# Optimization experiments

Hardware: AMD Instinct MI355X
Metric: run time of the kernel (lower is better)

Reference implementation:

```python
import jax, jax.numpy as jnp
import numpy as np

N_NODES, FEAT_DIM, EMBED_DIM, BATCH, N_NEIGH = 200000, 128, 64, 8192, 64


def setup_inputs() -> dict:
    key = jax.random.key(0)
    k0, k1, k2, k3, k4, k5 = jax.random.split(key, 6)
    return {
        "features_table": jax.random.normal(k0, (N_NODES, FEAT_DIM), jnp.float32),
        # xavier-uniform-like scale for [2*feat_dim, embed_dim]
        "weight": jax.random.normal(k1, (2 * FEAT_DIM, EMBED_DIM), jnp.float32)
        * (1.0 / np.sqrt(2 * FEAT_DIM)),
        "nodes": jax.random.randint(k2, (BATCH,), 0, N_NODES),
        "batch_scores": jax.random.normal(k3, (BATCH, 2), jnp.float32),
        "neigh_scores": jax.random.normal(k4, (BATCH, N_NEIGH, 2), jnp.float32),
        "neighs_ids": jax.random.randint(k5, (BATCH, N_NEIGH), 0, N_NODES),
        "num_sample": 16,
    }


def reference(features_table, weight, nodes, batch_scores, neigh_scores, neighs_ids, num_sample):
    # |center_score - neigh_score| per candidate neighbor  -> [B, K]
    score_diff = jnp.abs(batch_scores[:, :1] - neigh_scores[:, :, 0])
    # keep num_sample neighbors with SMALLEST score diff (top_k on negated diffs)
    neg_top, sel_idx = jax.lax.top_k(-score_diff, num_sample)  # [B, k]
    samp_scores = -neg_top  # selected (ascending-ish) score diffs, as in choose_step_test
    sel_ids = jnp.take_along_axis(neighs_ids, sel_idx, axis=1)  # [B, k]
    # masked-mean aggregation == mean of the k selected neighbor features
    neigh_feats = features_table[sel_ids]            # [B, k, F]
    agg_feats = neigh_feats.mean(axis=1)             # [B, F]
    self_feats = features_table[nodes]               # [B, F]
    cat_feats = jnp.concatenate([self_feats, agg_feats], axis=1)  # [B, 2F]
    to_feats = jax.nn.relu(cat_feats @ weight)       # [B, E]
    return to_feats, samp_scores
```

## Files before the change

### kernel.cpp

```cpp
#include <hip/hip_runtime.h>

#define BATCH   8192
#define NNEIGH  64
#define FEAT    128
#define EMBED   64
#define ROWS    8
#define CATP    260
#define EPAD    68
#define KCH     8

__global__ __launch_bounds__(256, 4) void intra_agg_kernel(
    const float* __restrict__ feat,
    const float* __restrict__ W,
    const int*   __restrict__ nodes,
    const float* __restrict__ bscore,
    const float* __restrict__ nscore,
    const int*   __restrict__ nids,
    const int*   __restrict__ ns_ptr,
    float*       __restrict__ out)
{
    const int b0   = blockIdx.x * ROWS;
    const int tid  = threadIdx.x;
    const int lane = tid & 63;
    const int wave = tid >> 6;
    const int ns   = *ns_ptr;

    __shared__ float s_cat[ROWS * CATP];
    __shared__ float s_part[KCH][ROWS][EPAD];

    const int r0   = wave * 2;
    const int half = lane >> 5;
    const int c    = lane & 31;

    const int    selfnode = nodes[b0 + r0 + half];
    const float4 self4    = *(const float4*)&feat[(size_t)selfnode * FEAT + c * 4];

    float d[2];
    int   idx[2];
    #pragma unroll
    for (int i = 0; i < 2; ++i) {
        const int row = b0 + r0 + i;
        const float  ctr = bscore[row * 2];
        const float2 sc  = *(const float2*)&nscore[(size_t)(row * NNEIGH + lane) * 2];
        d[i]   = fabsf(ctr - sc.x);
        idx[i] = lane;
    }
    #pragma unroll
    for (int k = 2; k <= 64; k <<= 1) {
        #pragma unroll
        for (int j = k >> 1; j > 0; j >>= 1) {
            #pragma unroll
            for (int i = 0; i < 2; ++i) {
                const float od = __shfl_xor(d[i], j);
                const int   oi = __shfl_xor(idx[i], j);
                const bool up    = ((lane & k) == 0);
                const bool lower = ((lane & j) == 0);
                const bool oless = (od < d[i]) || (od == d[i] && oi < idx[i]);
                if ((lower == up) ? oless : !oless) { d[i] = od; idx[i] = oi; }
            }
        }
    }
    int gid[2] = {0, 0};
    #pragma unroll
    for (int i = 0; i < 2; ++i) {
        const int row = b0 + r0 + i;
        if (lane < ns) {
            out[(size_t)BATCH * EMBED + (size_t)row * ns + lane] = d[i];
            gid[i] = nids[row * NNEIGH + idx[i]];
        }
    }

    float4 a = make_float4(0.f, 0.f, 0.f, 0.f);
    if (ns == 16) {
        #pragma unroll
        for (int j = 0; j < 16; ++j) {
            const int id0 = __shfl(gid[0], j);
            const int id1 = __shfl(gid[1], j);
            const int id  = half ? id1 : id0;
            const float4 v = *(const float4*)&feat[(size_t)id * FEAT + c * 4];
            a.x += v.x; a.y += v.y; a.z += v.z; a.w += v.w;
        }
    } else {
        for (int j = 0; j < ns; ++j) {
            const int id0 = __shfl(gid[0], j);
            const int id1 = __shfl(gid[1], j);
            const int id  = half ? id1 : id0;
            const float4 v = *(const float4*)&feat[(size_t)id * FEAT + c * 4];
            a.x += v.x; a.y += v.y; a.z += v.z; a.w += v.w;
        }
    }
    const float inv_ns = 1.0f / (float)ns;
    a.x *= inv_ns; a.y *= inv_ns; a.z *= inv_ns; a.w *= inv_ns;

    {
        const int r = r0 + half;
        *(float4*)&s_cat[r * CATP + c * 4]        = self4;
        *(float4*)&s_cat[r * CATP + FEAT + c * 4] = a;
    }
    __syncthreads();

    {
        const int q  = tid & 15;
        const int rq = (tid >> 4) & 1;
        const int ks = tid >> 5;
        const int k0 = ks * 32;

        float4 acc[4];
        #pragma unroll
        for (int r = 0; r < 4; ++r) acc[r] = make_float4(0.f, 0.f, 0.f, 0.f);

        #pragma unroll
        for (int kk = 0; kk < 32; kk += 4) {
            const int k = k0 + kk;
            float4 cv[4];
            #pragma unroll
            for (int r = 0; r < 4; ++r)
                cv[r] = *(const float4*)&s_cat[(rq * 4 + r) * CATP + k];
            #pragma unroll
            for (int t = 0; t < 4; ++t) {
                const float4 w4 = *(const float4*)&W[(size_t)(k + t) * EMBED + q * 4];
                #pragma unroll
                for (int r = 0; r < 4; ++r) {
                    const float cf = (t == 0) ? cv[r].x : (t == 1) ? cv[r].y
                                   : (t == 2) ? cv[r].z : cv[r].w;
                    acc[r].x += cf * w4.x; acc[r].y += cf * w4.y;
                    acc[r].z += cf * w4.z; acc[r].w += cf * w4.w;
                }
            }
        }
        #pragma unroll
        for (int r = 0; r < 4; ++r)
            *(float4*)&s_part[ks][rq * 4 + r][q * 4] = acc[r];
    }
    __syncthreads();

    if (tid < ROWS * 16) {
        const int r2 = tid >> 4;
        const int q  = tid & 15;
        float4 o = make_float4(0.f, 0.f, 0.f, 0.f);
        #pragma unroll
        for (int p = 0; p < KCH; ++p) {
            const float4 v = *(const float4*)&s_part[p][r2][q * 4];
            o.x += v.x; o.y += v.y; o.z += v.z; o.w += v.w;
        }
        o.x = fmaxf(o.x, 0.f); o.y = fmaxf(o.y, 0.f);
        o.z = fmaxf(o.z, 0.f); o.w = fmaxf(o.w, 0.f);
        *(float4*)&out[(size_t)(b0 + r2) * EMBED + q * 4] = o;
    }
}

extern "C" void kernel_launch(void* const* d_in, const int* in_sizes, int n_in,
                              void* d_out, int out_size, void* d_ws, size_t ws_size,
                              hipStream_t stream) {
    const float* feat   = (const float*)d_in[0];
    const float* W      = (const float*)d_in[1];
    const int*   nodes  = (const int*)d_in[2];
    const float* bscore = (const float*)d_in[3];
    const float* nscore = (const float*)d_in[4];
    const int*   nids   = (const int*)d_in[5];
    const int*   nsamp  = (const int*)d_in[6];
    float* out = (float*)d_out;

    intra_agg_kernel<<<BATCH / ROWS, 256, 0, stream>>>(feat, W, nodes, bscore,
                                                       nscore, nids, nsamp, out);
}
```

Baseline: 23.91 us.

## Replace bitonic sort with rank-by-counting selection and permute scatter

Swaps the 64-lane bitonic sort for a per-lane rank computed by comparing against all 63 other lanes through xor shuffles. Each lane then scatters its score straight to its rank slot, and the neighbor id is routed to that slot with ds_permute. Neighbor ids are now loaded up front, so the dependent gather after sorting goes away. This trades 21 compare-exchange stages, each with two shuffles per row, for 63 single-value shuffles per row.

```diff
diff --git a/kernel.cpp b/kernel.cpp
--- a/kernel.cpp
+++ b/kernel.cpp
@@ -31,60 +31,52 @@
     const int r0   = wave * 2;
     const int half = lane >> 5;
     const int c    = lane & 31;
+    const int rA   = b0 + r0;
+    const int rB   = rA + 1;
 
-    const int    selfnode = nodes[b0 + r0 + half];
+    const int    selfnode = nodes[rA + half];
     const float4 self4    = *(const float4*)&feat[(size_t)selfnode * FEAT + c * 4];
+    const int    nidA     = nids[rA * NNEIGH + lane];
+    const int    nidB     = nids[rB * NNEIGH + lane];
 
-    float d[2];
-    int   idx[2];
+    const float  ctrA = bscore[rA * 2];
+    const float  ctrB = bscore[rB * 2];
+    const float2 scA  = *(const float2*)&nscore[(size_t)(rA * NNEIGH + lane) * 2];
+    const float2 scB  = *(const float2*)&nscore[(size_t)(rB * NNEIGH + lane) * 2];
+    const float  dA   = fabsf(ctrA - scA.x);
+    const float  dB   = fabsf(ctrB - scB.x);
+
+    int rankA = 0, rankB = 0;
     #pragma unroll
-    for (int i = 0; i < 2; ++i) {
-        const int row = b0 + r0 + i;
-        const float  ctr = bscore[row * 2];
-        const float2 sc  = *(const float2*)&nscore[(size_t)(row * NNEIGH + lane) * 2];
-        d[i]   = fabsf(ctr - sc.x);
-        idx[i] = lane;
+    for (int m = 1; m < 64; ++m) {
+        const float oA = __shfl_xor(dA, m);
+        const float oB = __shfl_xor(dB, m);
+        const int   ol = lane ^ m;
+        rankA += (int)((oA < dA) | ((oA == dA) & (ol < lane)));
+        rankB += (int)((oB < dB) | ((oB == dB) & (ol < lane)));
     }
-    #pragma unroll
-    for (int k = 2; k <= 64; k <<= 1) {
-        #pragma unroll
-        for (int j = k >> 1; j > 0; j >>= 1) {
-            #pragma unroll
-            for (int i = 0; i < 2; ++i) {
-                const float od = __shfl_xor(d[i], j);
-                const int   oi = __shfl_xor(idx[i], j);
-                const bool up    = ((lane & k) == 0);
-                const bool lower = ((lane & j) == 0);
-                const bool oless = (od < d[i]) || (od == d[i] && oi < idx[i]);
-                if ((lower == up) ? oless : !oless) { d[i] = od; idx[i] = oi; }
-            }
-        }
-    }
-    int gid[2] = {0, 0};
-    #pragma unroll
-    for (int i = 0; i < 2; ++i) {
-        const int row = b0 + r0 + i;
-        if (lane < ns) {
-            out[(size_t)BATCH * EMBED + (size_t)row * ns + lane] = d[i];
-            gid[i] = nids[row * NNEIGH + idx[i]];
-        }
-    }
+
+    if (rankA < ns) out[(size_t)BATCH * EMBED + (size_t)rA * ns + rankA] = dA;
+    if (rankB < ns) out[(size_t)BATCH * EMBED + (size_t)rB * ns + rankB] = dB;
+
+    const int gidA = __builtin_amdgcn_ds_permute(rankA << 2, nidA);
+    const int gidB = __builtin_amdgcn_ds_permute(rankB << 2, nidB);
 
     float4 a = make_float4(0.f, 0.f, 0.f, 0.f);
     if (ns == 16) {
         #pragma unroll
         for (int j = 0; j < 16; ++j) {
-            const int id0 = __shfl(gid[0], j);
-            const int id1 = __shfl(gid[1], j);
-            const int id  = half ? id1 : id0;
+            const int iA = __shfl(gidA, j);
+            const int iB = __shfl(gidB, j);
+            const int id = half ? iB : iA;
             const float4 v = *(const float4*)&feat[(size_t)id * FEAT + c * 4];
             a.x += v.x; a.y += v.y; a.z += v.z; a.w += v.w;
         }
     } else {
         for (int j = 0; j < ns; ++j) {
-            const int id0 = __shfl(gid[0], j);
-            const int id1 = __shfl(gid[1], j);
-            const int id  = half ? id1 : id0;
+            const int iA = __shfl(gidA, j);
+            const int iB = __shfl(gidB, j);
+            const int id = half ? iB : iA;
             const float4 v = *(const float4*)&feat[(size_t)id * FEAT + c * 4];
             a.x += v.x; a.y += v.y; a.z += v.z; a.w += v.w;
         }
```

Measured after the change: 24.06 us. About the same (+0.7%).
